# Kernel optimization log

Hardware: AMD Instinct MI355X
Metric: run time of the kernel (lower is better)

The kernel has to match this reference:

```python
import jax, jax.numpy as jnp
import numpy as np

N = 100000      # nodes
E = 1600000     # edges
DIN, DH, DOUT = 128, 256, 40


def setup_inputs() -> dict:
    key = jax.random.key(0)
    ks = jax.random.split(key, 24)

    def w(i, fan_in, fan_out):
        s = 1.0 / np.sqrt(fan_in)
        return jax.random.uniform(ks[i], (fan_in, fan_out), jnp.float32, -s, s)

    def b(i, fan_in, fan_out):
        s = 1.0 / np.sqrt(fan_in)
        return jax.random.uniform(ks[i], (fan_out,), jnp.float32, -s, s)

    return {
        "x": jax.random.normal(ks[0], (N, DIN), jnp.float32),
        "edge_index": jax.random.randint(ks[1], (2, E), 0, N, dtype=jnp.int64),
        # updates_continues: Linear(DIN,DH), Linear(DH,DH), Linear(DH,DOUT)
        "Wc0": w(2, DIN, DH),  "bc0": b(3, DIN, DH),
        "Wc1": w(4, DH, DH),   "bc1": b(5, DH, DH),
        "Wc2": w(6, DH, DOUT), "bc2": b(7, DH, DOUT),
        # updates_exit: Linear(DIN,DOUT) x2, Linear(DH,DOUT) x2
        "We0": w(8, DIN, DOUT),  "be0": b(9, DIN, DOUT),
        "We1": w(10, DIN, DOUT), "be1": b(11, DIN, DOUT),
        "We2": w(12, DH, DOUT),  "be2": b(13, DH, DOUT),
        "We3": w(14, DH, DOUT),  "be3": b(15, DH, DOUT),
    }


def _gcn_agg(h, src, dst):
    """Symmetric-normalized GCN aggregation with self-loops: D^-1/2 (A+I) D^-1/2 h."""
    ones = jnp.ones(src.shape[0], h.dtype)
    deg = jax.ops.segment_sum(ones, dst, num_segments=N) + 1.0  # self-loop
    dinv = jax.lax.rsqrt(deg)
    coef = dinv[src] * dinv[dst]                    # [E]
    msgs = h[src] * coef[:, None]                   # [E, d] gather
    out = jax.ops.segment_sum(msgs, dst, num_segments=N)  # scatter-add
    return out + h * (dinv * dinv)[:, None]         # self-loop term


def reference(x, edge_index, Wc0, bc0, Wc1, bc1, Wc2, bc2,
              We0, be0, We1, be1, We2, be2, We3, be3):
    src, dst = edge_index[0], edge_index[1]
    Wc = [(Wc0, bc0), (Wc1, bc1), (Wc2, bc2)]
    We = [(We0, be0), (We1, be1), (We2, be2), (We3, be3)]

    h = x
    outs = [jax.nn.log_softmax(h @ We[0][0] + We[0][1], axis=1)]
    for i in range(3):
        h = _gcn_agg(h, src, dst)
        outs.append(jax.nn.log_softmax(h @ We[i + 1][0] + We[i + 1][1], axis=1))
        h = h @ Wc[i][0] + Wc[i][1]
        if i < 2:
            h = jax.nn.relu(h)  # dropout is identity in eval mode
    return jnp.stack(outs, axis=1)  # [N, num_layers+1, DOUT]
```

## Files before the change

kernel.cpp:

```cpp
#include <hip/hip_runtime.h>

#define NNODES 100000
#define NEDGES 1600000
#define NBKT 782

typedef __attribute__((ext_vector_type(8))) short bf16x8;
typedef __attribute__((ext_vector_type(4))) float f32x4;
typedef __attribute__((ext_vector_type(2))) float f32x2;

__device__ __forceinline__ float bf2f(unsigned v) {
  union { unsigned u; float f; } x; x.u = v << 16; return x.f;
}
__device__ __forceinline__ unsigned short f2bf(float f) {
  union { float f; unsigned u; } x; x.f = f;
  unsigned r = x.u + 0x7fffu + ((x.u >> 16) & 1u);
  return (unsigned short)(r >> 16);
}
__device__ __forceinline__ f32x2 unpk(unsigned u) {
  union { unsigned q; float f; } lo, hi;
  lo.q = u << 16; hi.q = u & 0xffff0000u;
  f32x2 r; r.x = lo.f; r.y = hi.f; return r;
}

__global__ void k_probe(const unsigned* __restrict__ xw, const int* __restrict__ ei,
                        int* __restrict__ flags, int* __restrict__ bcnt) {
  __shared__ int cF, cI;
  if (threadIdx.x == 0) { cF = 0; cI = 0; }
  __syncthreads();
  int t = threadIdx.x;
  int hf = 0;
  for (int i = t; i < 2048; i += 256) {
    unsigned lo = xw[i] & 0xffffu;
    unsigned e = (lo >> 7) & 0xffu;
    if (e >= 0xC0u) hf++;
  }
  atomicAdd(&cF, hf);
  int hi = 0;
  if (ei[2 * t + 1] != 0) hi++;
  atomicAdd(&cI, hi);
  for (int i = t; i < NBKT; i += 256) bcnt[i] = 0;
  __syncthreads();
  if (threadIdx.x == 0) {
    flags[0] = (cF > 32) ? 1 : 0;
    flags[1] = (cI < 16) ? 1 : 0;
  }
}

__device__ __forceinline__ int edge_at(const int* __restrict__ ei, int j, int i64) {
  return i64 ? ei[2 * j] : ei[j];
}

struct CvtParams {
  const void* src[13];
  unsigned short* dst[13];
  int n[13];
};

__global__ void k_cvt(CvtParams p, const int* __restrict__ flags,
                      const float* __restrict__ dinv, unsigned short* __restrict__ xs) {
  int a = blockIdx.y;
  int n = p.n[a];
  int f32 = flags[0];
  const float* sf = (const float*)p.src[a];
  const unsigned short* sb = (const unsigned short*)p.src[a];
  unsigned short* d = p.dst[a];
  for (int i = blockIdx.x * blockDim.x + threadIdx.x; i < n; i += gridDim.x * blockDim.x) {
    if (a == 0) {
      float v = f32 ? sf[i] : bf2f((unsigned)sb[i]);
      d[i] = f32 ? f2bf(v) : sb[i];
      xs[i] = f2bf(v * dinv[i >> 7]);
    } else {
      d[i] = f32 ? f2bf(sf[i]) : sb[i];
    }
  }
}

__global__ void k_wprep(const unsigned short* __restrict__ Wc0, unsigned short* __restrict__ WTc0,
                        const unsigned short* __restrict__ Wc1, unsigned short* __restrict__ WTc1,
                        const unsigned short* __restrict__ We0, unsigned short* __restrict__ WT40e0,
                        const unsigned short* __restrict__ We1, unsigned short* __restrict__ WT40e1,
                        const unsigned short* __restrict__ We2, unsigned short* __restrict__ WT40e2,
                        const unsigned short* __restrict__ We3, unsigned short* __restrict__ WT40e3) {
  int job = blockIdx.y;
  int idx = blockIdx.x * 256 + threadIdx.x;
  switch (job) {
    case 0: if (idx < 128 * 256) { int k = idx >> 8, c = idx & 255; WTc0[c * 128 + k] = Wc0[idx]; } break;
    case 1: if (idx < 256 * 256) { int k = idx >> 8, c = idx & 255; WTc1[c * 256 + k] = Wc1[idx]; } break;
    case 2: if (idx < 48 * 128) { int c = idx / 128, k = idx % 128; WT40e0[idx] = (c < 40) ? We0[k * 40 + c] : (unsigned short)0; } break;
    case 3: if (idx < 48 * 128) { int c = idx / 128, k = idx % 128; WT40e1[idx] = (c < 40) ? We1[k * 40 + c] : (unsigned short)0; } break;
    case 4: if (idx < 48 * 256) { int c = idx / 256, k = idx % 256; WT40e2[idx] = (c < 40) ? We2[k * 40 + c] : (unsigned short)0; } break;
    case 5: if (idx < 48 * 256) { int c = idx / 256, k = idx % 256; WT40e3[idx] = (c < 40) ? We3[k * 40 + c] : (unsigned short)0; } break;
  }
}


__global__ __launch_bounds__(256) void k_bcnt(const int* __restrict__ ei,
                                              int* __restrict__ bcnt,
                                              const int* __restrict__ flags) {
  __shared__ int h[NBKT];
  int t = threadIdx.x;
  for (int i = t; i < NBKT; i += 256) h[i] = 0;
  __syncthreads();
  int i64 = flags[1];
  int e0 = blockIdx.x * 4096;
#pragma unroll
  for (int k = 0; k < 16; ++k) {
    int e = e0 + t + k * 256;
    if (e < NEDGES) {
      int d = edge_at(ei, NEDGES + e, i64);
      if ((unsigned)d < NNODES) atomicAdd(&h[d >> 7], 1);
    }
  }
  __syncthreads();
  for (int i = t; i < NBKT; i += 256)
    if (h[i]) atomicAdd(&bcnt[i], h[i]);
}

__global__ void k_bscan2(const int* __restrict__ bcnt, int* __restrict__ bbase,
                         int* __restrict__ gcur) {
  int l = threadIdx.x;
  int v[13];
  int s = 0;
#pragma unroll
  for (int k = 0; k < 13; ++k) {
    int j = l * 13 + k;
    v[k] = (j < NBKT) ? bcnt[j] : 0;
    s += v[k];
  }
  int x = s;
#pragma unroll
  for (int o = 1; o < 64; o <<= 1) {
    int y = __shfl_up(x, o, 64);
    if (l >= o) x += y;
  }
  int excl = x - s;
#pragma unroll
  for (int k = 0; k < 13; ++k) {
    int j = l * 13 + k;
    if (j < NBKT) { bbase[j] = excl; gcur[j] = excl; }
    excl += v[k];
  }
  if (l == 63) bbase[NBKT] = x;
}

__global__ __launch_bounds__(256) void k_bstage(const int* __restrict__ ei,
                                                int* __restrict__ gcur,
                                                int* __restrict__ stage,
                                                const int* __restrict__ flags) {
  __shared__ int h[NBKT];
  __shared__ int base[NBKT];
  int t = threadIdx.x;
  for (int i = t; i < NBKT; i += 256) h[i] = 0;
  __syncthreads();
  int i64 = flags[1];
  int e0 = blockIdx.x * 4096;
  int bkt[16], lp[16], rec[16];
#pragma unroll
  for (int k = 0; k < 16; ++k) {
    bkt[k] = -1;
    int e = e0 + t + k * 256;
    if (e < NEDGES) {
      int d = edge_at(ei, NEDGES + e, i64);
      if ((unsigned)d < NNODES) {
        int s = edge_at(ei, e, i64);
        if ((unsigned)s >= NNODES) s = NNODES - 1;
        bkt[k] = d >> 7;
        rec[k] = ((d & 127) << 17) | s;
        lp[k] = atomicAdd(&h[bkt[k]], 1);
      }
    }
  }
  __syncthreads();
  for (int i = t; i < NBKT; i += 256)
    base[i] = h[i] ? atomicAdd(&gcur[i], h[i]) : 0;
  __syncthreads();
#pragma unroll
  for (int k = 0; k < 16; ++k)
    if (bkt[k] >= 0) stage[base[bkt[k]] + lp[k]] = rec[k];
}

__global__ __launch_bounds__(256) void k_bplace(const int* __restrict__ stage,
                                                const int* __restrict__ bbase,
                                                int* __restrict__ offs,
                                                float* __restrict__ dinv,
                                                int* __restrict__ csr_src) {
  __shared__ int h[128];
  __shared__ int cur[128];
  int b = blockIdx.x;
  int t = threadIdx.x;
  int n0 = b * 128;
  int NN = NNODES - n0; if (NN > 128) NN = 128;
  int s0 = bbase[b], s1 = bbase[b + 1];
  int cnt = s1 - s0;
  if (t < 128) h[t] = 0;
  __syncthreads();
  for (int i = t; i < cnt; i += 256) {
    int rec = stage[s0 + i];
    atomicAdd(&h[rec >> 17], 1);
  }
  __syncthreads();
  if (t < 64) {
    int a = h[2 * t], c = h[2 * t + 1];
    int s = a + c;
    int x = s;
#pragma unroll
    for (int o = 1; o < 64; o <<= 1) {
      int y = __shfl_up(x, o, 64);
      if (t >= o) x += y;
    }
    int excl = s0 + x - s;
    cur[2 * t] = excl;
    cur[2 * t + 1] = excl + a;
    if (2 * t < NN) {
      offs[n0 + 2 * t] = excl;
      dinv[n0 + 2 * t] = rsqrtf((float)a + 1.0f);
    }
    if (2 * t + 1 < NN) {
      offs[n0 + 2 * t + 1] = excl + a;
      dinv[n0 + 2 * t + 1] = rsqrtf((float)c + 1.0f);
    }
  }
  if (b == NBKT - 1 && t == 0) offs[NNODES] = s1;
  __syncthreads();
  for (int i = t; i < cnt; i += 256) {
    int rec = stage[s0 + i];
    int pos = atomicAdd(&cur[rec >> 17], 1);
    csr_src[pos] = rec & 0x1FFFF;
  }
}

__device__ __forceinline__ void accp(f32x2 (&acc)[4], uint4 u, float w) {
  acc[0] += unpk(u.x) * w;
  acc[1] += unpk(u.y) * w;
  acc[2] += unpk(u.z) * w;
  acc[3] += unpk(u.w) * w;
}

template <int D, int EPB>
__global__ __launch_bounds__(256) void k_agg(
    const unsigned short* __restrict__ hin, unsigned short* __restrict__ hout,
    const int* __restrict__ offs, const int* __restrict__ csr_src,
    const float* __restrict__ dinv) {
  constexpr int LPR = D / 8;
  constexpr int R = 64 / LPR;
  constexpr int NB = EPB / R;
  const int lane = threadIdx.x & 63;
  const int g = lane / LPR;
  const int l = lane % LPR;
  const int v = (blockIdx.x * 256 + threadIdx.x) >> 6;
  if (v >= NNODES) return;

  float dv = dinv[v];
  const size_t vbase = (size_t)v * D + l * 8;
  uint4 su = *(const uint4*)(hin + vbase);
  f32x2 acc[4];
#pragma unroll
  for (int k = 0; k < 4; ++k) acc[k] = (f32x2)0.f;
  accp(acc, su, (g == 0) ? 1.f : 0.f);

  int b0 = offs[v];
  int n = offs[v + 1] - b0;
  if (n > 0) {
    int s[NB];
    float wg[NB];
#pragma unroll
    for (int j = 0; j < NB; ++j) {
      int e = j * R + g;
      int ec = (e < n) ? e : (n - 1);
      s[j] = csr_src[b0 + ec];
      wg[j] = (e < n) ? 1.f : 0.f;
    }
    for (int i = 0; i < n; i += EPB) {
      uint4 gu[NB];
#pragma unroll
      for (int j = 0; j < NB; ++j)
        gu[j] = *(const uint4*)(hin + (size_t)s[j] * D + l * 8);
      float wc[NB];
#pragma unroll
      for (int j = 0; j < NB; ++j) wc[j] = wg[j];
      int i2 = i + EPB;
#pragma unroll
      for (int j = 0; j < NB; ++j) {
        int e = i2 + j * R + g;
        int ec = (e < n) ? e : (n - 1);
        s[j] = csr_src[b0 + ec];
        wg[j] = (e < n) ? 1.f : 0.f;
      }
#pragma unroll
      for (int j = 0; j < NB; ++j) accp(acc, gu[j], wc[j]);
    }
  }
  float a8[8];
#pragma unroll
  for (int k = 0; k < 4; ++k) { a8[2 * k] = acc[k].x; a8[2 * k + 1] = acc[k].y; }
#pragma unroll
  for (int k = 0; k < 8; ++k) {
#pragma unroll
    for (int o = LPR; o < 64; o <<= 1) a8[k] += __shfl_xor(a8[k], o, 64);
  }
  if (g == 0) {
    uint4 ov;
    ov.x = (unsigned)f2bf(dv * a8[0]) | ((unsigned)f2bf(dv * a8[1]) << 16);
    ov.y = (unsigned)f2bf(dv * a8[2]) | ((unsigned)f2bf(dv * a8[3]) << 16);
    ov.z = (unsigned)f2bf(dv * a8[4]) | ((unsigned)f2bf(dv * a8[5]) << 16);
    ov.w = (unsigned)f2bf(dv * a8[6]) | ((unsigned)f2bf(dv * a8[7]) << 16);
    *(uint4*)(hout + vbase) = ov;
  }
}

__global__ __launch_bounds__(256) void k_agg40(
    const unsigned short* __restrict__ P, const int* __restrict__ offs,
    const int* __restrict__ csr_src, const float* __restrict__ dinv,
    const unsigned short* __restrict__ bias, float* __restrict__ outp) {
  const int lane = threadIdx.x & 63;
  const int g = lane >> 5, l = lane & 31;
  const bool act = l < 20;
  const int v = (blockIdx.x * 256 + threadIdx.x) >> 6;
  if (v >= NNODES) return;

  float dv = dinv[v];
  f32x2 a = (f32x2)0.f;
  if (act && g == 0) a = unpk(*(const unsigned*)(P + (size_t)v * 40 + l * 2));
  int b0 = offs[v];
  int n = offs[v + 1] - b0;
  if (n > 0) {
    int s[4];
    float wg[4];
#pragma unroll
    for (int j = 0; j < 4; ++j) {
      int e = j * 2 + g;
      int ec = (e < n) ? e : (n - 1);
      s[j] = csr_src[b0 + ec];
      wg[j] = (e < n) ? 1.f : 0.f;
    }
    for (int i = 0; i < n; i += 8) {
      unsigned gu[4];
#pragma unroll
      for (int j = 0; j < 4; ++j)
        gu[j] = act ? *(const unsigned*)(P + (size_t)s[j] * 40 + l * 2) : 0u;
      float wc[4];
#pragma unroll
      for (int j = 0; j < 4; ++j) wc[j] = wg[j];
      int i2 = i + 8;
#pragma unroll
      for (int j = 0; j < 4; ++j) {
        int e = i2 + j * 2 + g;
        int ec = (e < n) ? e : (n - 1);
        s[j] = csr_src[b0 + ec];
        wg[j] = (e < n) ? 1.f : 0.f;
      }
#pragma unroll
      for (int j = 0; j < 4; ++j) a += unpk(gu[j]) * wc[j];
    }
  }
  a.x += __shfl_xor(a.x, 32, 64);
  a.y += __shfl_xor(a.y, 32, 64);
  float a0 = 0.f, a1 = 0.f;
  if (act) {
    a0 = dv * a.x + bf2f((unsigned)bias[l * 2]);
    a1 = dv * a.y + bf2f((unsigned)bias[l * 2 + 1]);
  }
  float m = act ? fmaxf(a0, a1) : -1e30f;
#pragma unroll
  for (int o = 16; o > 0; o >>= 1) m = fmaxf(m, __shfl_xor(m, o, 32));
  float ss = act ? (expf(a0 - m) + expf(a1 - m)) : 0.f;
#pragma unroll
  for (int o = 16; o > 0; o >>= 1) ss += __shfl_xor(ss, o, 32);
  float ls = logf(ss) + m;
  if (act && g == 0) {
    float2 o2;
    o2.x = a0 - ls;
    o2.y = a1 - ls;
    *(float2*)(outp + (size_t)v * 160 + l * 2) = o2;
  }
}

template <int K, bool SCALE>
__global__ __launch_bounds__(256) void k_mlp_mfma(
    const unsigned short* __restrict__ A, const unsigned short* __restrict__ WT,
    const unsigned short* __restrict__ bias, unsigned short* __restrict__ out,
    const float* __restrict__ dinv) {
  __shared__ short As[128 * 40];
  __shared__ short Bs[128 * 40];
  const int t = threadIdx.x;
  const int lane = t & 63, wv = t >> 6;
  const int m0 = blockIdx.x * 128;
  const int c0 = blockIdx.y * 128;
  const int mw = (wv >> 1) * 64, nw = (wv & 1) * 64;
  const int lr = lane & 15, lq = lane >> 4;

  f32x4 acc[4][4];
#pragma unroll
  for (int i = 0; i < 4; ++i)
#pragma unroll
    for (int j = 0; j < 4; ++j) acc[i][j] = (f32x4)0.f;

  for (int kc = 0; kc < K; kc += 32) {
    __syncthreads();
#pragma unroll
    for (int it = 0; it < 2; ++it) {
      int idx = t + it * 256;
      int row = idx >> 2, seg = idx & 3;
      uint4 u = make_uint4(0, 0, 0, 0);
      int gr = m0 + row;
      if (gr < NNODES) u = *(const uint4*)(A + (size_t)gr * K + kc + seg * 8);
      *(uint4*)&As[row * 40 + seg * 8] = u;
      uint4 v = *(const uint4*)(WT + (size_t)(c0 + row) * K + kc + seg * 8);
      *(uint4*)&Bs[row * 40 + seg * 8] = v;
    }
    __syncthreads();
    bf16x8 af[4], bfr[4];
#pragma unroll
    for (int i = 0; i < 4; ++i)
      af[i] = *(const bf16x8*)&As[(mw + 16 * i + lr) * 40 + lq * 8];
#pragma unroll
    for (int j = 0; j < 4; ++j)
      bfr[j] = *(const bf16x8*)&Bs[(nw + 16 * j + lr) * 40 + lq * 8];
#pragma unroll
    for (int i = 0; i < 4; ++i)
#pragma unroll
      for (int j = 0; j < 4; ++j)
        acc[i][j] = __builtin_amdgcn_mfma_f32_16x16x32_bf16(af[i], bfr[j], acc[i][j], 0, 0, 0);
  }

  float bv[4];
#pragma unroll
  for (int j = 0; j < 4; ++j) bv[j] = bf2f((unsigned)bias[c0 + nw + 16 * j + lr]);
#pragma unroll
  for (int i = 0; i < 4; ++i) {
    int rbase = m0 + mw + 16 * i + lq * 4;
#pragma unroll
    for (int r = 0; r < 4; ++r) {
      int row = rbase + r;
      if (row < NNODES) {
        float s = SCALE ? dinv[row] : 1.f;
#pragma unroll
        for (int j = 0; j < 4; ++j) {
          int col = c0 + nw + 16 * j + lr;
          float v = fmaxf(acc[i][j][r] + bv[j], 0.f) * s;
          out[(size_t)row * 256 + col] = f2bf(v);
        }
      }
    }
  }
}

template <int K, bool SOFTMAX>
__global__ __launch_bounds__(256) void k_exit_mfma(
    const unsigned short* __restrict__ A, const unsigned short* __restrict__ WT,
    const unsigned short* __restrict__ bias, float* __restrict__ outp,
    unsigned short* __restrict__ Pout, const float* __restrict__ dinv) {
  constexpr int KP = K + 8;
  __shared__ short As[128 * 40];
  __shared__ short Bs[48 * KP];
  const int t = threadIdx.x;
  const int lane = t & 63, wv = t >> 6;
  const int m0 = blockIdx.x * 128;
  const int mw = wv * 32;
  const int lr = lane & 15, lq = lane >> 4;

  for (int idx = t; idx < 48 * (K / 8); idx += 256) {
    int row = idx / (K / 8), seg = idx % (K / 8);
    uint4 w = *(const uint4*)(WT + (size_t)row * K + seg * 8);
    *(uint4*)&Bs[row * KP + seg * 8] = w;
  }

  f32x4 acc[2][3];
#pragma unroll
  for (int i = 0; i < 2; ++i)
#pragma unroll
    for (int j = 0; j < 3; ++j) acc[i][j] = (f32x4)0.f;

  for (int kc = 0; kc < K; kc += 32) {
    __syncthreads();
#pragma unroll
    for (int it = 0; it < 2; ++it) {
      int idx = t + it * 256;
      int row = idx >> 2, seg = idx & 3;
      uint4 u = make_uint4(0, 0, 0, 0);
      int gr = m0 + row;
      if (gr < NNODES) u = *(const uint4*)(A + (size_t)gr * K + kc + seg * 8);
      *(uint4*)&As[row * 40 + seg * 8] = u;
    }
    __syncthreads();
    bf16x8 af[2], bfr[3];
#pragma unroll
    for (int i = 0; i < 2; ++i)
      af[i] = *(const bf16x8*)&As[(mw + 16 * i + lr) * 40 + lq * 8];
#pragma unroll
    for (int j = 0; j < 3; ++j)
      bfr[j] = *(const bf16x8*)&Bs[(16 * j + lr) * KP + kc + lq * 8];
#pragma unroll
    for (int i = 0; i < 2; ++i)
#pragma unroll
      for (int j = 0; j < 3; ++j)
        acc[i][j] = __builtin_amdgcn_mfma_f32_16x16x32_bf16(af[i], bfr[j], acc[i][j], 0, 0, 0);
  }

  if (SOFTMAX) {
    float bv0 = bf2f((unsigned)bias[lr]);
    float bv1 = bf2f((unsigned)bias[16 + lr]);
    float bv2 = (lr < 8) ? bf2f((unsigned)bias[32 + lr]) : 0.f;
#pragma unroll
    for (int i = 0; i < 2; ++i) {
#pragma unroll
      for (int r = 0; r < 4; ++r) {
        int row = m0 + mw + 16 * i + lq * 4 + r;
        float v0 = acc[i][0][r] + bv0;
        float v1 = acc[i][1][r] + bv1;
        float v2 = (lr < 8) ? (acc[i][2][r] + bv2) : -1e30f;
        float m = fmaxf(fmaxf(v0, v1), v2);
#pragma unroll
        for (int o = 8; o > 0; o >>= 1) m = fmaxf(m, __shfl_xor(m, o, 16));
        float ss = expf(v0 - m) + expf(v1 - m) + ((lr < 8) ? expf(v2 - m) : 0.f);
#pragma unroll
        for (int o = 8; o > 0; o >>= 1) ss += __shfl_xor(ss, o, 16);
        float ls = logf(ss) + m;
        if (row < NNODES) {
          outp[(size_t)row * 160 + lr] = v0 - ls;
          outp[(size_t)row * 160 + 16 + lr] = v1 - ls;
          if (lr < 8) outp[(size_t)row * 160 + 32 + lr] = v2 - ls;
        }
      }
    }
  } else {
#pragma unroll
    for (int i = 0; i < 2; ++i) {
#pragma unroll
      for (int r = 0; r < 4; ++r) {
        int row = m0 + mw + 16 * i + lq * 4 + r;
        if (row < NNODES) {
          float s = dinv[row];
          Pout[(size_t)row * 40 + lr] = f2bf(acc[i][0][r] * s);
          Pout[(size_t)row * 40 + 16 + lr] = f2bf(acc[i][1][r] * s);
          if (lr < 8) Pout[(size_t)row * 40 + 32 + lr] = f2bf(acc[i][2][r] * s);
        }
      }
    }
  }
}

extern "C" void kernel_launch(void* const* d_in, const int* in_sizes, int n_in,
                              void* d_out, int out_size, void* d_ws, size_t ws_size,
                              hipStream_t stream) {
  const void* x_raw   = d_in[0];
  const int* ei       = (const int*)d_in[1];
  float* out          = (float*)d_out;

  char* ws = (char*)d_ws;
  int*   flags    = (int*)(ws + 0);
  int*   bcnt     = (int*)(ws + 4096);
  int*   gcur     = (int*)(ws + 8192);
  int*   bbase    = (int*)(ws + 12288);
  float* dinv     = (float*)(ws + 524288);
  int*   offs     = (int*)(ws + 1048576);
  int*   csr_src  = (int*)(ws + 2097152);
  int*   stage    = (int*)(ws + 8650752);
  unsigned short* xb = (unsigned short*)(ws + 16777216);
  unsigned short* wb = (unsigned short*)(ws + 45088768);
  unsigned short* hA = (unsigned short*)(ws + 48234496);
  unsigned short* hB = (unsigned short*)(ws + 100663296);
  unsigned short* xs = hB;
  unsigned short* P  = xb;

  unsigned short* Wc0 = wb + 0;
  unsigned short* bc0 = wb + 32768;
  unsigned short* Wc1 = wb + 33024;
  unsigned short* bc1 = wb + 98560;
  unsigned short* We0 = wb + 98816;
  unsigned short* be0 = wb + 103936;
  unsigned short* We1 = wb + 103976;
  unsigned short* be1 = wb + 109096;
  unsigned short* We2 = wb + 109136;
  unsigned short* be2 = wb + 119376;
  unsigned short* We3 = wb + 119416;
  unsigned short* be3 = wb + 129656;
  unsigned short* WTc0  = wb + 131072;
  unsigned short* WTc1  = wb + 163840;
  unsigned short* WT40e0 = wb + 229376;
  unsigned short* WT40e1 = wb + 235520;
  unsigned short* WT40e2 = wb + 241664;
  unsigned short* WT40e3 = wb + 253952;

  dim3 B(256);
  k_probe<<<dim3(1), B, 0, stream>>>((const unsigned*)x_raw, ei, flags, bcnt);

  k_bcnt<<<dim3(391), B, 0, stream>>>(ei, bcnt, flags);
  k_bscan2<<<dim3(1), dim3(64), 0, stream>>>(bcnt, bbase, gcur);
  k_bstage<<<dim3(391), B, 0, stream>>>(ei, gcur, stage, flags);
  k_bplace<<<dim3(NBKT), B, 0, stream>>>(stage, bbase, offs, dinv, csr_src);

  CvtParams p;
  const int srcIdx[13] = {0, 2, 3, 4, 5, 8, 9, 10, 11, 12, 13, 14, 15};
  unsigned short* dsts[13] = {xb, Wc0, bc0, Wc1, bc1, We0, be0, We1, be1, We2, be2, We3, be3};
  const int ns[13] = {NNODES * 128, 128 * 256, 256, 256 * 256, 256,
                      128 * 40, 40, 128 * 40, 40, 256 * 40, 40, 256 * 40, 40};
  for (int i = 0; i < 13; ++i) { p.src[i] = d_in[srcIdx[i]]; p.dst[i] = dsts[i]; p.n[i] = ns[i]; }
  k_cvt<<<dim3(1024, 13), B, 0, stream>>>(p, flags, dinv, xs);
  k_wprep<<<dim3(256, 6), B, 0, stream>>>(Wc0, WTc0, Wc1, WTc1, We0, WT40e0,
                                          We1, WT40e1, We2, WT40e2, We3, WT40e3);

  k_exit_mfma<128, true><<<dim3(782), B, 0, stream>>>(xb, WT40e0, be0, out + 0 * 40, nullptr, dinv);
  k_agg<128, 16><<<dim3(25000), B, 0, stream>>>(xs, hA, offs, csr_src, dinv);
  k_exit_mfma<128, true><<<dim3(782), B, 0, stream>>>(hA, WT40e1, be1, out + 1 * 40, nullptr, dinv);
  k_mlp_mfma<128, true><<<dim3(782, 2), B, 0, stream>>>(hA, WTc0, bc0, hB, dinv);
  k_agg<256, 8><<<dim3(25000), B, 0, stream>>>(hB, hA, offs, csr_src, dinv);
  k_exit_mfma<256, true><<<dim3(782), B, 0, stream>>>(hA, WT40e2, be2, out + 2 * 40, nullptr, dinv);
  k_mlp_mfma<256, false><<<dim3(782, 2), B, 0, stream>>>(hA, WTc1, bc1, hB, nullptr);
  k_exit_mfma<256, false><<<dim3(782), B, 0, stream>>>(hB, WT40e3, nullptr, nullptr, P, dinv);
  k_agg40<<<dim3(25000), B, 0, stream>>>(P, offs, csr_src, dinv, be3, out + 3 * 40);
}
```

Baseline: 636.8 us.

## Merge small kernels: fold probe into bcnt, fuse weight prep, co-launch exit and MLP

Removes the separate probe kernel. Float-format detection now runs in k_bcnt block 0, and the int64 check is redone per wavefront with a ballot. Weight transposition is folded into the conversion kernel as an extra grid row. Each exit head and the MLP GEMM that read the same activation now run as one launch with the block index picking the role. The goal is fewer kernel launches and less serialization between small kernels. In exchange it adds a k_zero launch and a redundant i64 probe in every block.

```diff
diff --git a/kernel.cpp b/kernel.cpp
--- a/kernel.cpp
+++ b/kernel.cpp
@@ -21,87 +21,45 @@
   lo.q = u << 16; hi.q = u & 0xffff0000u;
   f32x2 r; r.x = lo.f; r.y = hi.f; return r;
 }
-
-__global__ void k_probe(const unsigned* __restrict__ xw, const int* __restrict__ ei,
-                        int* __restrict__ flags, int* __restrict__ bcnt) {
-  __shared__ int cF, cI;
-  if (threadIdx.x == 0) { cF = 0; cI = 0; }
-  __syncthreads();
-  int t = threadIdx.x;
-  int hf = 0;
-  for (int i = t; i < 2048; i += 256) {
-    unsigned lo = xw[i] & 0xffffu;
-    unsigned e = (lo >> 7) & 0xffu;
-    if (e >= 0xC0u) hf++;
-  }
-  atomicAdd(&cF, hf);
-  int hi = 0;
-  if (ei[2 * t + 1] != 0) hi++;
-  atomicAdd(&cI, hi);
-  for (int i = t; i < NBKT; i += 256) bcnt[i] = 0;
-  __syncthreads();
-  if (threadIdx.x == 0) {
-    flags[0] = (cF > 32) ? 1 : 0;
-    flags[1] = (cI < 16) ? 1 : 0;
-  }
-}
-
+__device__ __forceinline__ unsigned short ldcv(const void* p, int i, int f32) {
+  return f32 ? f2bf(((const float*)p)[i]) : ((const unsigned short*)p)[i];
+}
+__device__ __forceinline__ int detect_i64(const int* __restrict__ ei) {
+  int lane = threadIdx.x & 63;
+  int hv = ei[2 * lane + 1];
+  unsigned long long nz = __ballot(hv != 0);
+  return (__popcll(nz) < 4) ? 1 : 0;
+}
 __device__ __forceinline__ int edge_at(const int* __restrict__ ei, int j, int i64) {
   return i64 ? ei[2 * j] : ei[j];
 }
 
-struct CvtParams {
-  const void* src[13];
-  unsigned short* dst[13];
-  int n[13];
-};
-
-__global__ void k_cvt(CvtParams p, const int* __restrict__ flags,
-                      const float* __restrict__ dinv, unsigned short* __restrict__ xs) {
-  int a = blockIdx.y;
-  int n = p.n[a];
-  int f32 = flags[0];
-  const float* sf = (const float*)p.src[a];
-  const unsigned short* sb = (const unsigned short*)p.src[a];
-  unsigned short* d = p.dst[a];
-  for (int i = blockIdx.x * blockDim.x + threadIdx.x; i < n; i += gridDim.x * blockDim.x) {
-    if (a == 0) {
-      float v = f32 ? sf[i] : bf2f((unsigned)sb[i]);
-      d[i] = f32 ? f2bf(v) : sb[i];
-      xs[i] = f2bf(v * dinv[i >> 7]);
-    } else {
-      d[i] = f32 ? f2bf(sf[i]) : sb[i];
-    }
-  }
-}
-
-__global__ void k_wprep(const unsigned short* __restrict__ Wc0, unsigned short* __restrict__ WTc0,
-                        const unsigned short* __restrict__ Wc1, unsigned short* __restrict__ WTc1,
-                        const unsigned short* __restrict__ We0, unsigned short* __restrict__ WT40e0,
-                        const unsigned short* __restrict__ We1, unsigned short* __restrict__ WT40e1,
-                        const unsigned short* __restrict__ We2, unsigned short* __restrict__ WT40e2,
-                        const unsigned short* __restrict__ We3, unsigned short* __restrict__ WT40e3) {
-  int job = blockIdx.y;
-  int idx = blockIdx.x * 256 + threadIdx.x;
-  switch (job) {
-    case 0: if (idx < 128 * 256) { int k = idx >> 8, c = idx & 255; WTc0[c * 128 + k] = Wc0[idx]; } break;
-    case 1: if (idx < 256 * 256) { int k = idx >> 8, c = idx & 255; WTc1[c * 256 + k] = Wc1[idx]; } break;
-    case 2: if (idx < 48 * 128) { int c = idx / 128, k = idx % 128; WT40e0[idx] = (c < 40) ? We0[k * 40 + c] : (unsigned short)0; } break;
-    case 3: if (idx < 48 * 128) { int c = idx / 128, k = idx % 128; WT40e1[idx] = (c < 40) ? We1[k * 40 + c] : (unsigned short)0; } break;
-    case 4: if (idx < 48 * 256) { int c = idx / 256, k = idx % 256; WT40e2[idx] = (c < 40) ? We2[k * 40 + c] : (unsigned short)0; } break;
-    case 5: if (idx < 48 * 256) { int c = idx / 256, k = idx % 256; WT40e3[idx] = (c < 40) ? We3[k * 40 + c] : (unsigned short)0; } break;
-  }
+__global__ void k_zero(int* __restrict__ p, int n) {
+  int v = blockIdx.x * blockDim.x + threadIdx.x;
+  if (v < n) p[v] = 0;
 }
 
 
 __global__ __launch_bounds__(256) void k_bcnt(const int* __restrict__ ei,
                                               int* __restrict__ bcnt,
-                                              const int* __restrict__ flags) {
+                                              const unsigned* __restrict__ xw,
+                                              int* __restrict__ flags) {
   __shared__ int h[NBKT];
+  __shared__ int cF;
   int t = threadIdx.x;
   for (int i = t; i < NBKT; i += 256) h[i] = 0;
-  __syncthreads();
-  int i64 = flags[1];
+  if (blockIdx.x == 0 && t == 0) cF = 0;
+  __syncthreads();
+  if (blockIdx.x == 0) {
+    int hf = 0;
+    for (int i = t; i < 2048; i += 256) {
+      unsigned lo = xw[i] & 0xffffu;
+      unsigned e = (lo >> 7) & 0xffu;
+      if (e >= 0xC0u) hf++;
+    }
+    atomicAdd(&cF, hf);
+  }
+  int i64 = detect_i64(ei);
   int e0 = blockIdx.x * 4096;
 #pragma unroll
   for (int k = 0; k < 16; ++k) {
@@ -114,6 +72,7 @@
   __syncthreads();
   for (int i = t; i < NBKT; i += 256)
     if (h[i]) atomicAdd(&bcnt[i], h[i]);
+  if (blockIdx.x == 0 && t == 0) flags[0] = (cF > 32) ? 1 : 0;
 }
 
 __global__ void k_bscan2(const int* __restrict__ bcnt, int* __restrict__ bbase,
@@ -145,14 +104,13 @@
 
 __global__ __launch_bounds__(256) void k_bstage(const int* __restrict__ ei,
                                                 int* __restrict__ gcur,
-                                                int* __restrict__ stage,
-                                                const int* __restrict__ flags) {
+                                                int* __restrict__ stage) {
   __shared__ int h[NBKT];
   __shared__ int base[NBKT];
   int t = threadIdx.x;
   for (int i = t; i < NBKT; i += 256) h[i] = 0;
   __syncthreads();
-  int i64 = flags[1];
+  int i64 = detect_i64(ei);
   int e0 = blockIdx.x * 4096;
   int bkt[16], lp[16], rec[16];
 #pragma unroll
@@ -229,6 +187,56 @@
   }
 }
 
+struct CvtP {
+  const void* src[7];
+  unsigned short* dst[7];
+  int n[7];
+  const void* W[6];
+  unsigned short* WT[6];
+};
+
+__global__ void k_cvt(CvtP p, const int* __restrict__ flags,
+                      const float* __restrict__ dinv, unsigned short* __restrict__ xs) {
+  int a = blockIdx.y;
+  int f32 = flags[0];
+  if (a < 7) {
+    int n = p.n[a];
+    const float* sf = (const float*)p.src[a];
+    const unsigned short* sb = (const unsigned short*)p.src[a];
+    unsigned short* d = p.dst[a];
+    for (int i = blockIdx.x * blockDim.x + threadIdx.x; i < n; i += gridDim.x * blockDim.x) {
+      if (a == 0) {
+        float v = f32 ? sf[i] : bf2f((unsigned)sb[i]);
+        d[i] = f32 ? f2bf(v) : sb[i];
+        xs[i] = f2bf(v * dinv[i >> 7]);
+      } else {
+        d[i] = f32 ? f2bf(sf[i]) : sb[i];
+      }
+    }
+  } else {
+    int g = blockIdx.x * 256 + threadIdx.x;
+    if (g < 32768) {
+      int k = g >> 8, c = g & 255;
+      p.WT[0][c * 128 + k] = ldcv(p.W[0], g, f32);
+    } else if (g < 98304) {
+      int l = g - 32768; int k = l >> 8, c = l & 255;
+      p.WT[1][c * 256 + k] = ldcv(p.W[1], l, f32);
+    } else if (g < 104448) {
+      int l = g - 98304; int c = l >> 7, k = l & 127;
+      p.WT[2][l] = (c < 40) ? ldcv(p.W[2], k * 40 + c, f32) : (unsigned short)0;
+    } else if (g < 110592) {
+      int l = g - 104448; int c = l >> 7, k = l & 127;
+      p.WT[3][l] = (c < 40) ? ldcv(p.W[3], k * 40 + c, f32) : (unsigned short)0;
+    } else if (g < 122880) {
+      int l = g - 110592; int c = l >> 8, k = l & 255;
+      p.WT[4][l] = (c < 40) ? ldcv(p.W[4], k * 40 + c, f32) : (unsigned short)0;
+    } else if (g < 135168) {
+      int l = g - 122880; int c = l >> 8, k = l & 255;
+      p.WT[5][l] = (c < 40) ? ldcv(p.W[5], k * 40 + c, f32) : (unsigned short)0;
+    }
+  }
+}
+
 __device__ __forceinline__ void accp(f32x2 (&acc)[4], uint4 u, float w) {
   acc[0] += unpk(u.x) * w;
   acc[1] += unpk(u.y) * w;
@@ -376,16 +384,15 @@
 }
 
 template <int K, bool SCALE>
-__global__ __launch_bounds__(256) void k_mlp_mfma(
+__device__ __forceinline__ void mlp_body(
+    char* smem, int m0, int c0,
     const unsigned short* __restrict__ A, const unsigned short* __restrict__ WT,
     const unsigned short* __restrict__ bias, unsigned short* __restrict__ out,
     const float* __restrict__ dinv) {
-  __shared__ short As[128 * 40];
-  __shared__ short Bs[128 * 40];
+  short* As = (short*)smem;
+  short* Bs = (short*)(smem + 10240);
   const int t = threadIdx.x;
   const int lane = t & 63, wv = t >> 6;
-  const int m0 = blockIdx.x * 128;
-  const int c0 = blockIdx.y * 128;
   const int mw = (wv >> 1) * 64, nw = (wv & 1) * 64;
   const int lr = lane & 15, lq = lane >> 4;
 
@@ -446,16 +453,16 @@
 }
 
 template <int K, bool SOFTMAX>
-__global__ __launch_bounds__(256) void k_exit_mfma(
+__device__ __forceinline__ void exit_body(
+    char* smem, int m0,
     const unsigned short* __restrict__ A, const unsigned short* __restrict__ WT,
     const unsigned short* __restrict__ bias, float* __restrict__ outp,
     unsigned short* __restrict__ Pout, const float* __restrict__ dinv) {
   constexpr int KP = K + 8;
-  __shared__ short As[128 * 40];
-  __shared__ short Bs[48 * KP];
+  short* As = (short*)smem;
+  short* Bs = (short*)(smem + 10240);
   const int t = threadIdx.x;
   const int lane = t & 63, wv = t >> 6;
-  const int m0 = blockIdx.x * 128;
   const int mw = wv * 32;
   const int lr = lane & 15, lq = lane >> 4;
 
@@ -537,6 +544,40 @@
         }
       }
     }
+  }
+}
+
+template <int K> struct ExitSM { static constexpr int B = 10240 + 48 * (K + 8) * 2; };
+
+__global__ __launch_bounds__(256) void k_exit0(
+    const unsigned short* __restrict__ A, const unsigned short* __restrict__ WT,
+    const unsigned short* __restrict__ bias, float* __restrict__ outp,
+    const float* __restrict__ dinv) {
+  __shared__ __align__(16) char smem[ExitSM<128>::B];
+  exit_body<128, true>(smem, blockIdx.x * 128, A, WT, bias, outp, nullptr, dinv);
+}
+
+__global__ __launch_bounds__(256) void k_exit3(
+    const unsigned short* __restrict__ A, const unsigned short* __restrict__ WT,
+    unsigned short* __restrict__ Pout, const float* __restrict__ dinv) {
+  __shared__ __align__(16) char smem[ExitSM<256>::B];
+  exit_body<256, false>(smem, blockIdx.x * 128, A, WT, nullptr, nullptr, Pout, dinv);
+}
+
+template <int K, bool MLPSCALE>
+__global__ __launch_bounds__(256) void k_exit_mlp(
+    const unsigned short* __restrict__ A,
+    const unsigned short* __restrict__ WTmlp, const unsigned short* __restrict__ bmlp,
+    unsigned short* __restrict__ outmlp,
+    const unsigned short* __restrict__ WTex, const unsigned short* __restrict__ bex,
+    float* __restrict__ outp, const float* __restrict__ dinv) {
+  constexpr int SM = (ExitSM<K>::B > 20480) ? ExitSM<K>::B : 20480;
+  __shared__ __align__(16) char smem[SM];
+  int bid = blockIdx.x;
+  if (bid < 1564) {
+    mlp_body<K, MLPSCALE>(smem, (bid >> 1) * 128, (bid & 1) * 128, A, WTmlp, bmlp, outmlp, dinv);
+  } else {
+    exit_body<K, true>(smem, (bid - 1564) * 128, A, WTex, bex, outp, nullptr, dinv);
   }
 }
 
@@ -563,17 +604,11 @@
   unsigned short* xs = hB;
   unsigned short* P  = xb;
 
-  unsigned short* Wc0 = wb + 0;
   unsigned short* bc0 = wb + 32768;
-  unsigned short* Wc1 = wb + 33024;
   unsigned short* bc1 = wb + 98560;
-  unsigned short* We0 = wb + 98816;
   unsigned short* be0 = wb + 103936;
-  unsigned short* We1 = wb + 103976;
   unsigned short* be1 = wb + 109096;
-  unsigned short* We2 = wb + 109136;
   unsigned short* be2 = wb + 119376;
-  unsigned short* We3 = wb + 119416;
   unsigned short* be3 = wb + 129656;
   unsigned short* WTc0  = wb + 131072;
   unsigned short* WTc1  = wb + 163840;
@@ -583,30 +618,29 @@
   unsigned short* WT40e3 = wb + 253952;
 
   dim3 B(256);
-  k_probe<<<dim3(1), B, 0, stream>>>((const unsigned*)x_raw, ei, flags, bcnt);
-
-  k_bcnt<<<dim3(391), B, 0, stream>>>(ei, bcnt, flags);
+  k_zero<<<dim3(4), B, 0, stream>>>(bcnt, NBKT);
+  k_bcnt<<<dim3(391), B, 0, stream>>>(ei, bcnt, (const unsigned*)x_raw, flags);
   k_bscan2<<<dim3(1), dim3(64), 0, stream>>>(bcnt, bbase, gcur);
-  k_bstage<<<dim3(391), B, 0, stream>>>(ei, gcur, stage, flags);
+  k_bstage<<<dim3(391), B, 0, stream>>>(ei, gcur, stage);
   k_bplace<<<dim3(NBKT), B, 0, stream>>>(stage, bbase, offs, dinv, csr_src);
 
-  CvtParams p;
-  const int srcIdx[13] = {0, 2, 3, 4, 5, 8, 9, 10, 11, 12, 13, 14, 15};
-  unsigned short* dsts[13] = {xb, Wc0, bc0, Wc1, bc1, We0, be0, We1, be1, We2, be2, We3, be3};
-  const int ns[13] = {NNODES * 128, 128 * 256, 256, 256 * 256, 256,
-                      128 * 40, 40, 128 * 40, 40, 256 * 40, 40, 256 * 40, 40};
-  for (int i = 0; i < 13; ++i) { p.src[i] = d_in[srcIdx[i]]; p.dst[i] = dsts[i]; p.n[i] = ns[i]; }
-  k_cvt<<<dim3(1024, 13), B, 0, stream>>>(p, flags, dinv, xs);
-  k_wprep<<<dim3(256, 6), B, 0, stream>>>(Wc0, WTc0, Wc1, WTc1, We0, WT40e0,
-                                          We1, WT40e1, We2, WT40e2, We3, WT40e3);
-
-  k_exit_mfma<128, true><<<dim3(782), B, 0, stream>>>(xb, WT40e0, be0, out + 0 * 40, nullptr, dinv);
+  CvtP p;
+  const int bsrc[7] = {0, 3, 5, 9, 11, 13, 15};
+  unsigned short* bdst[7] = {xb, bc0, bc1, be0, be1, be2, be3};
+  const int bn[7] = {NNODES * 128, 256, 256, 40, 40, 40, 40};
+  for (int i = 0; i < 7; ++i) { p.src[i] = d_in[bsrc[i]]; p.dst[i] = bdst[i]; p.n[i] = bn[i]; }
+  const int wsrc[6] = {2, 4, 8, 10, 12, 14};
+  unsigned short* wdst[6] = {WTc0, WTc1, WT40e0, WT40e1, WT40e2, WT40e3};
+  for (int i = 0; i < 6; ++i) { p.W[i] = d_in[wsrc[i]]; p.WT[i] = wdst[i]; }
+  k_cvt<<<dim3(1024, 8), B, 0, stream>>>(p, flags, dinv, xs);
+
+  k_exit0<<<dim3(782), B, 0, stream>>>(xb, WT40e0, be0, out + 0 * 40, dinv);
   k_agg<128, 16><<<dim3(25000), B, 0, stream>>>(xs, hA, offs, csr_src, dinv);
-  k_exit_mfma<128, true><<<dim3(782), B, 0, stream>>>(hA, WT40e1, be1, out + 1 * 40, nullptr, dinv);
-  k_mlp_mfma<128, true><<<dim3(782, 2), B, 0, stream>>>(hA, WTc0, bc0, hB, dinv);
+  k_exit_mlp<128, true><<<dim3(2346), B, 0, stream>>>(hA, WTc0, bc0, hB,
+                                                      WT40e1, be1, out + 1 * 40, dinv);
   k_agg<256, 8><<<dim3(25000), B, 0, stream>>>(hB, hA, offs, csr_src, dinv);
-  k_exit_mfma<256, true><<<dim3(782), B, 0, stream>>>(hA, WT40e2, be2, out + 2 * 40, nullptr, dinv);
-  k_mlp_mfma<256, false><<<dim3(782, 2), B, 0, stream>>>(hA, WTc1, bc1, hB, nullptr);
-  k_exit_mfma<256, false><<<dim3(782), B, 0, stream>>>(hB, WT40e3, nullptr, nullptr, P, dinv);
+  k_exit_mlp<256, false><<<dim3(2346), B, 0, stream>>>(hA, WTc1, bc1, hB,
+                                                       WT40e2, be2, out + 2 * 40, dinv);
+  k_exit3<<<dim3(782), B, 0, stream>>>(hB, WT40e3, P, dinv);
   k_agg40<<<dim3(25000), B, 0, stream>>>(P, offs, csr_src, dinv, be3, out + 3 * 40);
 }
```

Measured after the change: 623.3 us, median of 2. 2.1% less time.
